# Performance work log

Measured on AMD Instinct MI355X. Metric: run time of the kernel, lower is better.

## Reference

```python
import jax, jax.numpy as jnp
import numpy as np

N, E, A, D, B = 30000, 60000, 6, 16, 4096
F_IN, F_HID, F_EMB = 256, 256, 256
ALPHA = 0.2  # LeakyReLU negative slope


def _layer(node_embs, edge_embs, edge_list, node_list, Wn, We, ae, an, concat):
    out = Wn.shape[1]
    hn = node_embs @ Wn                      # [N, out]
    he = edge_embs @ We                      # [E, out]
    # stage 1: hyperedge update = attention over its member nodes
    gn = hn[edge_list]                       # [E, A, out] gather
    se = (he @ ae[:out])[:, None] + gn @ ae[out:]            # [E, A]
    att_e = jax.nn.softmax(jax.nn.leaky_relu(se, ALPHA), axis=1)
    new_edge = jnp.einsum('ea,eao->eo', att_e, gn)           # [E, out]
    # stage 2: node update = attention over its incident hyperedges
    ge = new_edge[node_list]                 # [N, D, out] gather
    sn = (hn @ an[:out])[:, None] + ge @ an[out:]            # [N, D]
    att_n = jax.nn.softmax(jax.nn.leaky_relu(sn, ALPHA), axis=1)
    new_node = jnp.einsum('nd,ndo->no', att_n, ge)           # [N, out]
    if concat:
        return jax.nn.elu(new_node), jax.nn.elu(new_edge)
    return new_node, new_edge


def setup_inputs() -> dict:
    key = jax.random.key(0)
    ks = jax.random.split(key, 16)
    s = 0.1
    return {
        'batch_inputs': jax.random.randint(ks[0], (B, A + 1), 0, N),
        'node_embs': jax.random.normal(ks[1], (N, F_IN), jnp.float32),
        'edge_embs': jax.random.normal(ks[2], (E, F_IN), jnp.float32),
        'edge_list': jax.random.randint(ks[3], (E, A), 0, N),
        'node_list': jax.random.randint(ks[4], (N, D), 0, E),
        'Wn1': jax.random.normal(ks[5], (F_IN, F_HID), jnp.float32) * s,
        'We1': jax.random.normal(ks[6], (F_IN, F_HID), jnp.float32) * s,
        'ae1': jax.random.normal(ks[7], (2 * F_HID,), jnp.float32) * s,
        'an1': jax.random.normal(ks[8], (2 * F_HID,), jnp.float32) * s,
        'Wn2': jax.random.normal(ks[9], (F_HID, F_EMB), jnp.float32) * s,
        'We2': jax.random.normal(ks[10], (F_HID, F_EMB), jnp.float32) * s,
        'ae2': jax.random.normal(ks[11], (2 * F_EMB,), jnp.float32) * s,
        'an2': jax.random.normal(ks[12], (2 * F_EMB,), jnp.float32) * s,
    }


def reference(batch_inputs, node_embs, edge_embs, edge_list, node_list,
              Wn1, We1, ae1, an1, Wn2, We2, ae2, an2):
    # single attention head (nheads=1), concat=True -> ELU; dropout identity (eval)
    n1, e1 = _layer(node_embs, edge_embs, edge_list, node_list, Wn1, We1, ae1, an1, True)
    n2, e2 = _layer(n1, e1, edge_list, node_list, Wn2, We2, ae2, an2, False)
    n2, e2 = jax.nn.elu(n2), jax.nn.elu(e2)
    # assemble: slot 0 = hyperedge embedding, slots 1..right-1 = node embeddings
    S = batch_inputs.shape[1]
    cols = jnp.arange(S - 1)
    nz = batch_inputs[:, :-1] != 0
    right = jnp.max(jnp.where(nz, cols, -1), axis=1) + 1      # [B]
    pos = jnp.arange(S)
    mask = (pos[None, :] >= 1) & (pos[None, :] < right[:, None])  # [B, S]
    gathered = n2[batch_inputs]                               # [B, S, F_EMB]
    out = jnp.where(mask[:, :, None], gathered, jnp.float32(0))
    out = out.at[:, 0, :].set(e2[batch_inputs[:, 0]])
    return out
```

## Files before the change

### kernel.cpp

```cpp
#include <hip/hip_runtime.h>
#include <stdint.h>

typedef unsigned short u16;
typedef unsigned int   u32;
typedef __attribute__((ext_vector_type(8))) short bf16x8;
typedef __attribute__((ext_vector_type(4))) float f32x4;

#define N_NODES 30000
#define N_EDGES 60000
#define A_DEG   6
#define D_DEG   16
#define BATCH   4096
#define FEAT    256
#define APAD    8

__device__ __forceinline__ float bfbits2f(u32 hi){ union{u32 u; float f;} v; v.u = hi; return v.f; }
__device__ __forceinline__ float bf2f(u16 h){ return bfbits2f(((u32)h)<<16); }
__device__ __forceinline__ u16 f2bf(float f){
  union{float f; u32 u;} v; v.f = f;
  u32 u = v.u;
  return (u16)((u + 0x7fffu + ((u>>16)&1u)) >> 16);
}

struct F4 { float x,y,z,w; };
struct F8 { float v[8]; };

__device__ __forceinline__ F4 load4(const float* p){
  float4 t = *reinterpret_cast<const float4*>(p);
  F4 f; f.x=t.x; f.y=t.y; f.z=t.z; f.w=t.w; return f;
}
__device__ __forceinline__ F4 load4(const u16* p){
  uint2 u = *reinterpret_cast<const uint2*>(p);
  F4 f;
  f.x = bfbits2f(u.x<<16);
  f.y = bfbits2f(u.x & 0xffff0000u);
  f.z = bfbits2f(u.y<<16);
  f.w = bfbits2f(u.y & 0xffff0000u);
  return f;
}
__device__ __forceinline__ F8 load8(const float* p){
  float4 a = *reinterpret_cast<const float4*>(p);
  float4 b = *reinterpret_cast<const float4*>(p+4);
  F8 f; f.v[0]=a.x; f.v[1]=a.y; f.v[2]=a.z; f.v[3]=a.w;
        f.v[4]=b.x; f.v[5]=b.y; f.v[6]=b.z; f.v[7]=b.w; return f;
}
__device__ __forceinline__ F8 load8(const u16* p){
  uint4 u = *reinterpret_cast<const uint4*>(p);
  F8 f;
  f.v[0]=bfbits2f(u.x<<16); f.v[1]=bfbits2f(u.x&0xffff0000u);
  f.v[2]=bfbits2f(u.y<<16); f.v[3]=bfbits2f(u.y&0xffff0000u);
  f.v[4]=bfbits2f(u.z<<16); f.v[5]=bfbits2f(u.z&0xffff0000u);
  f.v[6]=bfbits2f(u.w<<16); f.v[7]=bfbits2f(u.w&0xffff0000u);
  return f;
}
__device__ __forceinline__ void acc8(float* o, uint4 u, float ww){
  o[0] += ww*bfbits2f(u.x<<16); o[1] += ww*bfbits2f(u.x&0xffff0000u);
  o[2] += ww*bfbits2f(u.y<<16); o[3] += ww*bfbits2f(u.y&0xffff0000u);
  o[4] += ww*bfbits2f(u.z<<16); o[5] += ww*bfbits2f(u.z&0xffff0000u);
  o[6] += ww*bfbits2f(u.w<<16); o[7] += ww*bfbits2f(u.w&0xffff0000u);
}
__device__ __forceinline__ void store_bf8(u16* p, const float* f){
  uint4 u;
  u.x = (u32)f2bf(f[0]) | ((u32)f2bf(f[1])<<16);
  u.y = (u32)f2bf(f[2]) | ((u32)f2bf(f[3])<<16);
  u.z = (u32)f2bf(f[4]) | ((u32)f2bf(f[5])<<16);
  u.w = (u32)f2bf(f[6]) | ((u32)f2bf(f[7])<<16);
  *reinterpret_cast<uint4*>(p) = u;
}

__device__ __forceinline__ float eluf(float x){ return x > 0.f ? x : (__expf(x) - 1.f); }
__device__ __forceinline__ float lrelu(float x){ return x > 0.f ? x : 0.2f*x; }

__device__ __forceinline__ float wave_sum_lane0(float v){
  #pragma unroll
  for (int off = 32; off > 0; off >>= 1) v += __shfl_down(v, off, 64);
  return v;
}
__device__ __forceinline__ float half_sum_all(float v){
  #pragma unroll
  for (int off = 1; off < 32; off <<= 1) v += __shfl_xor(v, off, 64);
  return v;
}

__global__ __launch_bounds__(256) void prep_k(
    const float* __restrict__ Wn1, u16* __restrict__ Wt1,
    const float* __restrict__ Wn2, u16* __restrict__ Wt2,
    const float* __restrict__ We1, const float* __restrict__ ae1, float* __restrict__ wE1,
    const float* __restrict__ We2, const float* __restrict__ ae2, float* __restrict__ wE2)
{
  if (blockIdx.z < 2){
    const float* W = blockIdx.z ? Wn2 : Wn1;
    u16* Wt        = blockIdx.z ? Wt2 : Wt1;
    __shared__ float T[32][33];
    const int bx = blockIdx.x;
    const int by = blockIdx.y;
    const int tc = threadIdx.x & 31;
    const int tr = threadIdx.x >> 5;
    #pragma unroll
    for (int i=0;i<4;i++){
      int r = tr + i*8;
      T[r][tc] = W[(bx*32 + r)*FEAT + by*32 + tc];
    }
    __syncthreads();
    #pragma unroll
    for (int i=0;i<4;i++){
      int r = tr + i*8;
      Wt[(by*32 + r)*FEAT + bx*32 + tc] = f2bf(T[tc][r]);
    }
  } else {
    const int vb   = blockIdx.y*8 + blockIdx.x;
    const int lane = threadIdx.x & 63;
    const int row  = vb*4 + (threadIdx.x >> 6);
    const int c    = lane*4;
    {
      F4 h = load4(We1 + (long)row*FEAT + c);
      F4 a = load4(ae1 + c);
      float p = wave_sum_lane0(h.x*a.x + h.y*a.y + h.z*a.z + h.w*a.w);
      if (lane == 0) wE1[row] = p;
    }
    {
      F4 h = load4(We2 + (long)row*FEAT + c);
      F4 a = load4(ae2 + c);
      float p = wave_sum_lane0(h.x*a.x + h.y*a.y + h.z*a.z + h.w*a.w);
      if (lane == 0) wE2[row] = p;
    }
  }
}

__global__ __launch_bounds__(256) void gemm_mfma_k(
    const float* __restrict__ X, const u16* __restrict__ Wt,
    const float* __restrict__ v1, const float* __restrict__ v2,
    u16* __restrict__ Y, float* __restrict__ hg, float* __restrict__ snb,
    int M)
{
  __shared__ u16 As[64][FEAT + APAD];
  __shared__ float hgs[64], sns[64];
  const int tid = threadIdx.x;
  const long row0 = (long)blockIdx.x * 64;

  if (tid < 64){ hgs[tid] = 0.f; sns[tid] = 0.f; }

  {
    const int c = (tid & 15) << 4;
    #pragma unroll
    for (int i=0;i<4;i++){
      const int r = (tid >> 4) + 16*i;
      u16* dst = &As[r][c];
      if (row0 + r < M){
        const float* src = X + (row0 + r)*FEAT + c;
        #pragma unroll
        for (int j=0;j<4;j++){
          F4 v = load4(src + 4*j);
          dst[4*j+0]=f2bf(v.x); dst[4*j+1]=f2bf(v.y);
          dst[4*j+2]=f2bf(v.z); dst[4*j+3]=f2bf(v.w);
        }
      } else {
        #pragma unroll
        for (int j=0;j<16;j++) dst[j] = 0;
      }
    }
  }
  __syncthreads();

  const int wave = tid >> 6;
  const int lane = tid & 63;
  const int l15  = lane & 15;
  const int kg   = lane >> 4;

  f32x4 acc[4][4] = {};

  for (int k0 = 0; k0 < FEAT; k0 += 32){
    bf16x8 a[4], b[4];
    #pragma unroll
    for (int rt=0;rt<4;rt++)
      a[rt] = *reinterpret_cast<const bf16x8*>(&As[rt*16 + l15][k0 + kg*8]);
    #pragma unroll
    for (int t=0;t<4;t++){
      const int n = wave*64 + t*16 + l15;
      b[t] = *reinterpret_cast<const bf16x8*>(Wt + (long)n*FEAT + k0 + kg*8);
    }
    #pragma unroll
    for (int rt=0;rt<4;rt++)
      #pragma unroll
      for (int t=0;t<4;t++)
        acc[rt][t] = __builtin_amdgcn_mfma_f32_16x16x32_bf16(a[rt], b[t], acc[rt][t], 0, 0, 0);
  }

  __syncthreads();

  float p1[4][4] = {}, p2[4][4] = {};
  #pragma unroll
  for (int t=0;t<4;t++){
    const int col = wave*64 + t*16 + l15;
    const float a1 = v1[col];
    const float a2 = v2[col];
    #pragma unroll
    for (int rt=0;rt<4;rt++){
      #pragma unroll
      for (int r=0;r<4;r++){
        const float val = acc[rt][t][r];
        As[rt*16 + kg*4 + r][col] = f2bf(val);
        p1[rt][r] += val * a1;
        p2[rt][r] += val * a2;
      }
    }
  }
  #pragma unroll
  for (int off=1; off<16; off<<=1){
    #pragma unroll
    for (int rt=0;rt<4;rt++)
      #pragma unroll
      for (int r=0;r<4;r++){
        p1[rt][r] += __shfl_xor(p1[rt][r], off, 64);
        p2[rt][r] += __shfl_xor(p2[rt][r], off, 64);
      }
  }
  if (l15 == 0){
    #pragma unroll
    for (int rt=0;rt<4;rt++)
      #pragma unroll
      for (int r=0;r<4;r++){
        atomicAdd(&hgs[rt*16 + kg*4 + r], p1[rt][r]);
        atomicAdd(&sns[rt*16 + kg*4 + r], p2[rt][r]);
      }
  }
  __syncthreads();

  {
    const int c = (tid & 15) << 4;
    #pragma unroll
    for (int i=0;i<4;i++){
      const int r = (tid >> 4) + 16*i;
      if (row0 + r < M){
        const uint4* s = reinterpret_cast<const uint4*>(&As[r][c]);
        uint4* d = reinterpret_cast<uint4*>(Y + (row0 + r)*FEAT + c);
        d[0] = s[0]; d[1] = s[1];
      }
    }
  }
  if (tid < 64 && row0 + tid < M){
    hg[row0 + tid]  = hgs[tid];
    snb[row0 + tid] = sns[tid];
  }
}

__global__ __launch_bounds__(256) void node_gemm_k(
    const u16* __restrict__ NE, const int* __restrict__ node_list,
    const float* __restrict__ snb1, const float* __restrict__ ned,
    const u16* __restrict__ Wt,
    const float* __restrict__ v1, const float* __restrict__ v2,
    u16* __restrict__ Y, float* __restrict__ hg, float* __restrict__ snb2,
    int M)
{
  __shared__ u16 As[64][FEAT + APAD];
  __shared__ float hgs[64], sns[64];
  const int tid = threadIdx.x;
  const long row0 = (long)blockIdx.x * 64;

  if (tid < 64){ hgs[tid] = 0.f; sns[tid] = 0.f; }

  const int hw = tid >> 5;
  const int hl = tid & 31;
  const int c  = hl*8;
  #pragma unroll
  for (int i=0;i<8;i++){
    const int r = hw*8 + i;
    const long n = row0 + r;
    u16* dst = &As[r][c];
    if (n < M){
      int idx[D_DEG];
      #pragma unroll
      for (int d=0; d<D_DEG; d++) idx[d] = node_list[n*D_DEG + d];
      float nv[D_DEG];
      #pragma unroll
      for (int d=0; d<D_DEG; d++) nv[d] = ned[idx[d]];
      const float sb = snb1[n];
      float w[D_DEG];
      float mx = -1e30f;
      #pragma unroll
      for (int d=0; d<D_DEG; d++){
        float s = lrelu(sb + nv[d]);
        w[d] = s; mx = fmaxf(mx, s);
      }
      float sum = 0.f;
      #pragma unroll
      for (int d=0; d<D_DEG; d++){ w[d] = __expf(w[d]-mx); sum += w[d]; }
      const float inv = 1.f/sum;

      uint4 hb[D_DEG];
      #pragma unroll
      for (int d=0; d<D_DEG; d++)
        hb[d] = *reinterpret_cast<const uint4*>(NE + (long)idx[d]*FEAT + c);
      float o[8] = {};
      #pragma unroll
      for (int d=0; d<D_DEG; d++) acc8(o, hb[d], w[d]*inv);

      #pragma unroll
      for (int j=0;j<8;j++) dst[j] = f2bf(eluf(o[j]));
    } else {
      #pragma unroll
      for (int j=0;j<8;j++) dst[j] = 0;
    }
  }
  __syncthreads();

  const int wave = tid >> 6;
  const int lane = tid & 63;
  const int l15  = lane & 15;
  const int kg   = lane >> 4;

  f32x4 acc[4][4] = {};

  for (int k0 = 0; k0 < FEAT; k0 += 32){
    bf16x8 a[4], b[4];
    #pragma unroll
    for (int rt=0;rt<4;rt++)
      a[rt] = *reinterpret_cast<const bf16x8*>(&As[rt*16 + l15][k0 + kg*8]);
    #pragma unroll
    for (int t=0;t<4;t++){
      const int n = wave*64 + t*16 + l15;
      b[t] = *reinterpret_cast<const bf16x8*>(Wt + (long)n*FEAT + k0 + kg*8);
    }
    #pragma unroll
    for (int rt=0;rt<4;rt++)
      #pragma unroll
      for (int t=0;t<4;t++)
        acc[rt][t] = __builtin_amdgcn_mfma_f32_16x16x32_bf16(a[rt], b[t], acc[rt][t], 0, 0, 0);
  }

  __syncthreads();

  float p1[4][4] = {}, p2[4][4] = {};
  #pragma unroll
  for (int t=0;t<4;t++){
    const int col = wave*64 + t*16 + l15;
    const float a1 = v1[col];
    const float a2 = v2[col];
    #pragma unroll
    for (int rt=0;rt<4;rt++){
      #pragma unroll
      for (int r=0;r<4;r++){
        const float val = acc[rt][t][r];
        As[rt*16 + kg*4 + r][col] = f2bf(val);
        p1[rt][r] += val * a1;
        p2[rt][r] += val * a2;
      }
    }
  }
  #pragma unroll
  for (int off=1; off<16; off<<=1){
    #pragma unroll
    for (int rt=0;rt<4;rt++)
      #pragma unroll
      for (int r=0;r<4;r++){
        p1[rt][r] += __shfl_xor(p1[rt][r], off, 64);
        p2[rt][r] += __shfl_xor(p2[rt][r], off, 64);
      }
  }
  if (l15 == 0){
    #pragma unroll
    for (int rt=0;rt<4;rt++)
      #pragma unroll
      for (int r=0;r<4;r++){
        atomicAdd(&hgs[rt*16 + kg*4 + r], p1[rt][r]);
        atomicAdd(&sns[rt*16 + kg*4 + r], p2[rt][r]);
      }
  }
  __syncthreads();

  {
    const int cc = (tid & 15) << 4;
    #pragma unroll
    for (int i=0;i<4;i++){
      const int r = (tid >> 4) + 16*i;
      if (row0 + r < M){
        const uint4* s = reinterpret_cast<const uint4*>(&As[r][cc]);
        uint4* d = reinterpret_cast<uint4*>(Y + (row0 + r)*FEAT + cc);
        d[0] = s[0]; d[1] = s[1];
      }
    }
  }
  if (tid < 64 && row0 + tid < M){
    hg[row0 + tid]   = hgs[tid];
    snb2[row0 + tid] = sns[tid];
  }
}

template<bool SB_PRE, bool SEB_OUT>
__global__ __launch_bounds__(256) void edge_attn_k(const u16* __restrict__ Hn,
    const float* __restrict__ Xe, const float* __restrict__ wE,
    const int* __restrict__ edge_list,
    const float* __restrict__ hg, const float* __restrict__ an_hi,
    const float* __restrict__ seb_in, const float* __restrict__ wE_nxt,
    float* __restrict__ seb_out,
    u16* __restrict__ NE, float* __restrict__ ned)
{
  const int tid = threadIdx.x;
  const int hl  = tid & 31;
  const int e   = blockIdx.x*8 + (tid >> 5);
  const int c   = hl*8;

  int idx[A_DEG];
  #pragma unroll
  for (int a=0;a<A_DEG;a++) idx[a] = edge_list[e*A_DEG + a];
  float hgv[A_DEG];
  #pragma unroll
  for (int a=0;a<A_DEG;a++) hgv[a] = hg[idx[a]];
  uint4 hb[A_DEG];
  #pragma unroll
  for (int a=0;a<A_DEG;a++)
    hb[a] = *reinterpret_cast<const uint4*>(Hn + (long)idx[a]*FEAT + c);

  float sb;
  if (SB_PRE){
    sb = seb_in[e];
  } else {
    F8 x = load8(Xe + (long)e*FEAT + c);
    F8 v = load8(wE + c);
    float p = 0.f;
    #pragma unroll
    for (int j=0;j<8;j++) p += x.v[j]*v.v[j];
    sb = half_sum_all(p);
  }

  float w[A_DEG];
  float mx = -1e30f;
  #pragma unroll
  for (int a=0;a<A_DEG;a++){
    float s = lrelu(sb + hgv[a]);
    w[a] = s; mx = fmaxf(mx, s);
  }
  float sum = 0.f;
  #pragma unroll
  for (int a=0;a<A_DEG;a++){ w[a] = __expf(w[a]-mx); sum += w[a]; }
  const float inv = 1.f/sum;

  float o[8] = {};
  #pragma unroll
  for (int a=0;a<A_DEG;a++) acc8(o, hb[a], w[a]*inv);
  store_bf8(NE + (long)e*FEAT + c, o);

  {
    F8 v = load8(an_hi + c);
    float p = 0.f;
    #pragma unroll
    for (int j=0;j<8;j++) p += o[j]*v.v[j];
    p = half_sum_all(p);
    if (hl == 0) ned[e] = p;
  }
  if (SEB_OUT){
    F8 v = load8(wE_nxt + c);
    float p = 0.f;
    #pragma unroll
    for (int j=0;j<8;j++) p += eluf(bf2f(f2bf(o[j])))*v.v[j];
    p = half_sum_all(p);
    if (hl == 0) seb_out[e] = p;
  }
}

__global__ __launch_bounds__(256) void node_assemble_k(
    const u16* __restrict__ NE, const int* __restrict__ node_list,
    const float* __restrict__ snb, const float* __restrict__ ned,
    const int* __restrict__ batch, float* __restrict__ out)
{
  const int b   = blockIdx.x;
  const int tid = threadIdx.x;
  const int hw  = tid >> 5;
  const int hl  = tid & 31;
  const int c   = hl*8;

  int right = 0;
  #pragma unroll
  for (int cc=0; cc<6; cc++){ if (batch[b*7 + cc] != 0) right = cc+1; }

  if (hw == 6){
    const int e = batch[b*7 + 0];
    F8 x = load8(NE + (long)e*FEAT + c);
    float4 o0, o1;
    o0.x=eluf(x.v[0]); o0.y=eluf(x.v[1]); o0.z=eluf(x.v[2]); o0.w=eluf(x.v[3]);
    o1.x=eluf(x.v[4]); o1.y=eluf(x.v[5]); o1.z=eluf(x.v[6]); o1.w=eluf(x.v[7]);
    float* po = out + ((long)b*7 + 0)*FEAT + c;
    *reinterpret_cast<float4*>(po)   = o0;
    *reinterpret_cast<float4*>(po+4) = o1;
  } else if (hw < 6){
    const int s  = hw + 1;
    float* po = out + ((long)b*7 + s)*FEAT + c;
    if (s < right){
      const int n = batch[b*7 + s];
      int idx[D_DEG];
      #pragma unroll
      for (int d=0; d<D_DEG; d++) idx[d] = node_list[(long)n*D_DEG + d];
      float nv[D_DEG];
      #pragma unroll
      for (int d=0; d<D_DEG; d++) nv[d] = ned[idx[d]];
      const float sb = snb[n];
      float w[D_DEG];
      float mx = -1e30f;
      #pragma unroll
      for (int d=0; d<D_DEG; d++){
        float sc = lrelu(sb + nv[d]);
        w[d] = sc; mx = fmaxf(mx, sc);
      }
      float sum = 0.f;
      #pragma unroll
      for (int d=0; d<D_DEG; d++){ w[d] = __expf(w[d]-mx); sum += w[d]; }
      const float inv = 1.f/sum;

      uint4 hb[D_DEG];
      #pragma unroll
      for (int d=0; d<D_DEG; d++)
        hb[d] = *reinterpret_cast<const uint4*>(NE + (long)idx[d]*FEAT + c);
      float o[8] = {};
      #pragma unroll
      for (int d=0; d<D_DEG; d++) acc8(o, hb[d], w[d]*inv);

      float4 o0, o1;
      o0.x=eluf(o[0]); o0.y=eluf(o[1]); o0.z=eluf(o[2]); o0.w=eluf(o[3]);
      o1.x=eluf(o[4]); o1.y=eluf(o[5]); o1.z=eluf(o[6]); o1.w=eluf(o[7]);
      *reinterpret_cast<float4*>(po)   = o0;
      *reinterpret_cast<float4*>(po+4) = o1;
    } else {
      float4 z; z.x=0.f; z.y=0.f; z.z=0.f; z.w=0.f;
      *reinterpret_cast<float4*>(po)   = z;
      *reinterpret_cast<float4*>(po+4) = z;
    }
  }
}

extern "C" void kernel_launch(void* const* d_in, const int* in_sizes, int n_in,
                              void* d_out, int out_size, void* d_ws, size_t ws_size,
                              hipStream_t stream)
{
  const int*   batch      = (const int*)d_in[0];
  const float* node_embs  = (const float*)d_in[1];
  const float* edge_embs  = (const float*)d_in[2];
  const int*   edge_list  = (const int*)d_in[3];
  const int*   node_list  = (const int*)d_in[4];
  const float* Wn1 = (const float*)d_in[5];
  const float* We1 = (const float*)d_in[6];
  const float* ae1 = (const float*)d_in[7];
  const float* an1 = (const float*)d_in[8];
  const float* Wn2 = (const float*)d_in[9];
  const float* We2 = (const float*)d_in[10];
  const float* ae2 = (const float*)d_in[11];
  const float* an2 = (const float*)d_in[12];
  float* out = (float*)d_out;

  char* ws = (char*)d_ws;
  size_t off = 0;
  auto alloc = [&](size_t bytes)->void* {
    void* p = ws + off; off += (bytes + 255) & ~(size_t)255; return p;
  };
  u16* bHn = (u16*)alloc((size_t)N_NODES*FEAT*2);
  u16* bNE = (u16*)alloc((size_t)N_EDGES*FEAT*2);
  u16* Wt1 = (u16*)alloc((size_t)FEAT*FEAT*2);
  u16* Wt2 = (u16*)alloc((size_t)FEAT*FEAT*2);
  float* hg   = (float*)alloc((size_t)N_NODES*4);
  float* snb  = (float*)alloc((size_t)N_NODES*4);
  float* ned  = (float*)alloc((size_t)N_EDGES*4);
  float* seb2 = (float*)alloc((size_t)N_EDGES*4);
  float* wE1  = (float*)alloc(FEAT*4);
  float* wE2  = (float*)alloc(FEAT*4);

  dim3 blk(256);
  const int gemm_grid = (N_NODES + 63) / 64;

  prep_k<<<dim3(8,8,3), blk, 0, stream>>>(Wn1, Wt1, Wn2, Wt2,
      We1, ae1, wE1, We2, ae2, wE2);

  gemm_mfma_k<<<gemm_grid, blk, 0, stream>>>(node_embs, Wt1,
      ae1+FEAT, an1, bHn, hg, snb, N_NODES);
  edge_attn_k<false,true><<<N_EDGES/8, blk, 0, stream>>>(bHn, edge_embs, wE1,
      edge_list, hg, an1+FEAT, nullptr, wE2, seb2, bNE, ned);

  node_gemm_k<<<gemm_grid, blk, 0, stream>>>(bNE, node_list, snb, ned,
      Wt2, ae2+FEAT, an2, bHn, hg, snb, N_NODES);

  edge_attn_k<true,false><<<N_EDGES/8, blk, 0, stream>>>(bHn, nullptr, nullptr,
      edge_list, hg, an2+FEAT, seb2, nullptr, nullptr, bNE, ned);

  node_assemble_k<<<BATCH, blk, 0, stream>>>(bNE, node_list, snb, ned, batch, out);
}
```

Measured before the change: 285.1 us.

## Move layer-1 edge score projection into GEMM launch as extra blocks

The layer-1 edge score (edge_embs dot wE1) is moved out of the first edge attention kernel and computed by extra blocks appended to the node GEMM grid, which write it to a new seb1 buffer. The edge attention kernel then reads a precomputed scalar per edge in both layers and no longer streams the 60000x256 fp32 edge_embs. This lets the memory-bound edge-embedding read overlap with the compute-bound MFMA GEMM instead of running serially inside the gather kernel. The cost is an extra 240 KB buffer write and read, plus a heavier first launch.

```diff
diff --git a/kernel.cpp b/kernel.cpp
--- a/kernel.cpp
+++ b/kernel.cpp
@@ -13,6 +13,8 @@
 #define BATCH   4096
 #define FEAT    256
 #define APAD    8
+#define GEMM_GRID ((N_NODES + 63) / 64)
+#define SB_GRID   (N_EDGES / 8)
 
 __device__ __forceinline__ float bfbits2f(u32 hi){ union{u32 u; float f;} v; v.u = hi; return v.f; }
 __device__ __forceinline__ float bf2f(u16 h){ return bfbits2f(((u32)h)<<16); }
@@ -127,15 +129,33 @@
   }
 }
 
-__global__ __launch_bounds__(256) void gemm_mfma_k(
+__global__ __launch_bounds__(256) void gemm_sb_k(
     const float* __restrict__ X, const u16* __restrict__ Wt,
     const float* __restrict__ v1, const float* __restrict__ v2,
     u16* __restrict__ Y, float* __restrict__ hg, float* __restrict__ snb,
-    int M)
+    int M,
+    const float* __restrict__ Xe, const float* __restrict__ wEv,
+    float* __restrict__ seb)
 {
   __shared__ u16 As[64][FEAT + APAD];
   __shared__ float hgs[64], sns[64];
   const int tid = threadIdx.x;
+
+  if (blockIdx.x >= GEMM_GRID){
+    const int eb = blockIdx.x - GEMM_GRID;
+    const int hl = tid & 31;
+    const int e  = eb*8 + (tid >> 5);
+    const int c  = hl*8;
+    F8 x = load8(Xe + (long)e*FEAT + c);
+    F8 v = load8(wEv + c);
+    float p = 0.f;
+    #pragma unroll
+    for (int j=0;j<8;j++) p += x.v[j]*v.v[j];
+    p = half_sum_all(p);
+    if (hl == 0) seb[e] = p;
+    return;
+  }
+
   const long row0 = (long)blockIdx.x * 64;
 
   if (tid < 64){ hgs[tid] = 0.f; sns[tid] = 0.f; }
@@ -386,9 +406,8 @@
   }
 }
 
-template<bool SB_PRE, bool SEB_OUT>
+template<bool SEB_OUT>
 __global__ __launch_bounds__(256) void edge_attn_k(const u16* __restrict__ Hn,
-    const float* __restrict__ Xe, const float* __restrict__ wE,
     const int* __restrict__ edge_list,
     const float* __restrict__ hg, const float* __restrict__ an_hi,
     const float* __restrict__ seb_in, const float* __restrict__ wE_nxt,
@@ -411,17 +430,7 @@
   for (int a=0;a<A_DEG;a++)
     hb[a] = *reinterpret_cast<const uint4*>(Hn + (long)idx[a]*FEAT + c);
 
-  float sb;
-  if (SB_PRE){
-    sb = seb_in[e];
-  } else {
-    F8 x = load8(Xe + (long)e*FEAT + c);
-    F8 v = load8(wE + c);
-    float p = 0.f;
-    #pragma unroll
-    for (int j=0;j<8;j++) p += x.v[j]*v.v[j];
-    sb = half_sum_all(p);
-  }
+  const float sb = seb_in[e];
 
   float w[A_DEG];
   float mx = -1e30f;
@@ -558,25 +567,27 @@
   float* hg   = (float*)alloc((size_t)N_NODES*4);
   float* snb  = (float*)alloc((size_t)N_NODES*4);
   float* ned  = (float*)alloc((size_t)N_EDGES*4);
+  float* seb1 = (float*)alloc((size_t)N_EDGES*4);
   float* seb2 = (float*)alloc((size_t)N_EDGES*4);
   float* wE1  = (float*)alloc(FEAT*4);
   float* wE2  = (float*)alloc(FEAT*4);
 
   dim3 blk(256);
-  const int gemm_grid = (N_NODES + 63) / 64;
 
   prep_k<<<dim3(8,8,3), blk, 0, stream>>>(Wn1, Wt1, Wn2, Wt2,
       We1, ae1, wE1, We2, ae2, wE2);
 
-  gemm_mfma_k<<<gemm_grid, blk, 0, stream>>>(node_embs, Wt1,
-      ae1+FEAT, an1, bHn, hg, snb, N_NODES);
-  edge_attn_k<false,true><<<N_EDGES/8, blk, 0, stream>>>(bHn, edge_embs, wE1,
-      edge_list, hg, an1+FEAT, nullptr, wE2, seb2, bNE, ned);
-
-  node_gemm_k<<<gemm_grid, blk, 0, stream>>>(bNE, node_list, snb, ned,
+  gemm_sb_k<<<GEMM_GRID + SB_GRID, blk, 0, stream>>>(node_embs, Wt1,
+      ae1+FEAT, an1, bHn, hg, snb, N_NODES,
+      edge_embs, wE1, seb1);
+
+  edge_attn_k<true><<<N_EDGES/8, blk, 0, stream>>>(bHn,
+      edge_list, hg, an1+FEAT, seb1, wE2, seb2, bNE, ned);
+
+  node_gemm_k<<<GEMM_GRID, blk, 0, stream>>>(bNE, node_list, snb, ned,
       Wt2, ae2+FEAT, an2, bHn, hg, snb, N_NODES);
 
-  edge_attn_k<true,false><<<N_EDGES/8, blk, 0, stream>>>(bHn, nullptr, nullptr,
+  edge_attn_k<false><<<N_EDGES/8, blk, 0, stream>>>(bHn,
       edge_list, hg, an2+FEAT, seb2, nullptr, nullptr, bNE, ned);
 
   node_assemble_k<<<BATCH, blk, 0, stream>>>(bNE, node_list, snb, ned, batch, out);
```

New measurement: 284.1 us. Within noise of the previous version (-0.4%).
